# Kernel tuning notes

Measured on AMD Instinct MI355X. Metric: run time of the kernel, lower is better.

The kernel has to match this reference:

```python
import jax, jax.numpy as jnp
import numpy as np

N_COLS = 4096
N_ROWS = 4096
H = 64          # args.hidden1
S = 2           # per-edge supp feature count (cv_supp/vc_supp dim 0)
S_VO = 2        # vo_supp feature dim
S_CO = 2        # co_supp feature dim
EDGE_DENSITY = 0.03


def setup_inputs() -> dict:
    key = jax.random.key(0)
    ks = jax.random.split(key, 20)
    col_hidden = jax.random.normal(ks[0], (N_COLS, H), jnp.float32)
    row_hidden = jax.random.normal(ks[1], (N_ROWS, H), jnp.float32)
    obj_hidden = jax.random.normal(ks[2], (1, H), jnp.float32)
    # sparse bipartite adjacency encoded in supp[0] != 0 (as in the TF code)
    mask = jax.random.bernoulli(ks[3], EDGE_DENSITY, (N_ROWS, N_COLS))
    cv_supp = jax.random.normal(ks[4], (S, N_ROWS, N_COLS), jnp.float32) * mask[None]
    vc_supp = jnp.transpose(cv_supp, (0, 2, 1))  # [S, ncols, nrows]
    vo_supp = jax.random.normal(ks[5], (N_COLS, S_VO), jnp.float32)
    co_supp = jax.random.normal(ks[6], (N_ROWS, S_CO), jnp.float32)
    w = 0.05
    W_vo = jax.random.normal(ks[7], (2 * H, H), jnp.float32) * w
    W_oc = jax.random.normal(ks[8], (2 * H, H), jnp.float32) * w
    W_vc = jax.random.normal(ks[9], (2 * H, H), jnp.float32) * w
    W_co = jax.random.normal(ks[10], (2 * H, H), jnp.float32) * w
    W_ov = jax.random.normal(ks[11], (2 * H, H), jnp.float32) * w
    W_cv = jax.random.normal(ks[12], (2 * H, H), jnp.float32) * w
    # attention scorer nets: Dense(concat_dim -> 1) + sigmoid
    w_attn_vo = jax.random.normal(ks[13], (2 * H + S_VO, 1), jnp.float32) * 0.1
    b_attn_vo = jnp.zeros((), jnp.float32)
    w_attn_co = jax.random.normal(ks[14], (2 * H + S_CO, 1), jnp.float32) * 0.1
    b_attn_co = jnp.zeros((), jnp.float32)
    # pairwise attn nets decomposed into [col | supp | row] weight slices
    w_cv_col = jax.random.normal(ks[15], (H,), jnp.float32) * 0.1
    w_cv_supp = jax.random.normal(ks[16], (S,), jnp.float32) * 0.1
    w_cv_row = jax.random.normal(ks[17], (H,), jnp.float32) * 0.1
    b_cv = jnp.zeros((), jnp.float32)
    w_vc_row = jax.random.normal(ks[18], (H,), jnp.float32) * 0.1
    w_vc_supp = jax.random.normal(ks[19], (S,), jnp.float32) * 0.1
    w_vc_col = jax.random.normal(jax.random.fold_in(key, 99), (H,), jnp.float32) * 0.1
    b_vc = jnp.zeros((), jnp.float32)
    return dict(col_hidden=col_hidden, row_hidden=row_hidden, obj_hidden=obj_hidden,
                cv_supp=cv_supp, vc_supp=vc_supp, vo_supp=vo_supp, co_supp=co_supp,
                W_vo=W_vo, W_oc=W_oc, W_vc=W_vc, W_co=W_co, W_ov=W_ov, W_cv=W_cv,
                w_attn_vo=w_attn_vo, b_attn_vo=b_attn_vo,
                w_attn_co=w_attn_co, b_attn_co=b_attn_co,
                w_cv_col=w_cv_col, w_cv_supp=w_cv_supp, w_cv_row=w_cv_row, b_cv=b_cv,
                w_vc_row=w_vc_row, w_vc_supp=w_vc_supp, w_vc_col=w_vc_col, b_vc=b_vc)


def _forward(col_hidden, row_hidden, obj_hidden, cv_supp, vc_supp, vo_supp, co_supp,
             W_vo, W_oc, W_vc, W_co, W_ov, W_cv,
             w_attn_vo, b_attn_vo, w_attn_co, b_attn_co,
             w_cv_col, w_cv_supp, w_cv_row, b_cv,
             w_vc_row, w_vc_supp, w_vc_col, b_vc):
    act = jax.nn.relu
    ncols, nrows = col_hidden.shape[0], row_hidden.shape[0]
    # ---- v -> o: attend over all columns, update obj node ----
    vo_in = jnp.concatenate([col_hidden, vo_supp,
                             jnp.broadcast_to(obj_hidden, (ncols, H))], axis=1)
    a_vo = jax.nn.sigmoid(vo_in @ w_attn_vo + b_attn_vo)          # [ncols, 1]
    v_o_out = a_vo.T @ col_hidden                                  # [1, H]
    obj = act(jnp.concatenate([obj_hidden, v_o_out], axis=1) @ W_vo)
    # ---- v -> c: per-row ragged neighbor attention, vectorized via masked pairwise scores ----
    nbr_cv = cv_supp[0] != 0                                       # [nrows, ncols]
    logits_cv = ((row_hidden @ w_cv_row)[:, None]
                 + (col_hidden @ w_cv_col)[None, :]
                 + jnp.einsum('snc,s->nc', cv_supp, w_cv_supp) + b_cv)
    score_cv = jnp.where(nbr_cv, jax.nn.sigmoid(logits_cv), 0.0)   # [nrows, ncols]
    v_out = score_cv @ col_hidden                                  # [nrows, H]
    o_c_out = act(jnp.concatenate([jnp.broadcast_to(obj, (nrows, H)), row_hidden], axis=1) @ W_oc)
    row_next = act(jnp.concatenate([o_c_out, v_out], axis=1) @ W_vc)
    # ---- c -> o ----
    co_in = jnp.concatenate([row_next, co_supp,
                             jnp.broadcast_to(obj, (nrows, H))], axis=1)
    a_co = jax.nn.sigmoid(co_in @ w_attn_co + b_attn_co)           # [nrows, 1]
    c_o_out = a_co.T @ row_next                                    # [1, H]
    obj = act(jnp.concatenate([obj, c_o_out], axis=1) @ W_co)
    # ---- c -> v ----
    nbr_vc = vc_supp[0] != 0                                       # [ncols, nrows]
    logits_vc = ((col_hidden @ w_vc_col)[:, None]
                 + (row_next @ w_vc_row)[None, :]
                 + jnp.einsum('scn,s->cn', vc_supp, w_vc_supp) + b_vc)
    score_vc = jnp.where(nbr_vc, jax.nn.sigmoid(logits_vc), 0.0)   # [ncols, nrows]
    c_out = score_vc @ row_next                                    # [ncols, H]
    o_v_out = act(jnp.concatenate([jnp.broadcast_to(obj, (ncols, H)), col_hidden], axis=1) @ W_ov)
    col_next = act(jnp.concatenate([o_v_out, c_out], axis=1) @ W_cv)
    return col_next, row_next, obj


def reference(col_hidden, row_hidden, obj_hidden, cv_supp, vc_supp, vo_supp, co_supp,
              W_vo, W_oc, W_vc, W_co, W_ov, W_cv,
              w_attn_vo, b_attn_vo, w_attn_co, b_attn_co,
              w_cv_col, w_cv_supp, w_cv_row, b_cv,
              w_vc_row, w_vc_supp, w_vc_col, b_vc):
    col_next, row_next, obj = _forward(
        col_hidden, row_hidden, obj_hidden, cv_supp, vc_supp, vo_supp, co_supp,
        W_vo, W_oc, W_vc, W_co, W_ov, W_cv,
        w_attn_vo, b_attn_vo, w_attn_co, b_attn_co,
        w_cv_col, w_cv_supp, w_cv_row, b_cv,
        w_vc_row, w_vc_supp, w_vc_col, b_vc)
    # original layer also passes the supp tensors through unchanged
    return (col_next, row_next, obj, cv_supp, vc_supp, vo_supp, co_supp)
```

## Files before the change

### kernel.cpp

```cpp
#include <hip/hip_runtime.h>
#include <math.h>

typedef float f4 __attribute__((ext_vector_type(4)));

#define PLANE (4096*4096)

#define OUT_COL 0
#define OUT_ROW 262144
#define OUT_OBJ 524288
#define OUT_CV  524352
#define OUT_VC  34078784
#define OUT_VO  67633216
#define OUT_CO  67641408

#define WS_VOACC 0
#define WS_COACC 64
#define WS_OBJ1  128
#define WS_RDCV  256
#define WS_CDCV  4352
#define WS_RDVC  8448
#define WS_CDVC  12544
#define WS_VOUT  16640
#define WS_COUT  278784
#define WS_PART  540928

__device__ __forceinline__ float sigf(float x) {
    return 1.0f / (1.0f + __expf(-x));
}

__global__ __launch_bounds__(256) void k_dots(
    const float* __restrict__ col_hidden, const float* __restrict__ row_hidden,
    const float* __restrict__ w_cv_col, const float* __restrict__ w_vc_col,
    const float* __restrict__ w_cv_row,
    float* __restrict__ cdcv, float* __restrict__ cdvc, float* __restrict__ rdcv)
{
    const int gw = blockIdx.x * 4 + (threadIdx.x >> 6);
    const int lane = threadIdx.x & 63;
    const int which = gw >> 12;
    const int row = gw & 4095;
    const float* x; const float* w; float* dst;
    if (which == 0)      { x = col_hidden; w = w_cv_col; dst = cdcv; }
    else if (which == 1) { x = col_hidden; w = w_vc_col; dst = cdvc; }
    else                 { x = row_hidden; w = w_cv_row; dst = rdcv; }
    float v = x[row * 64 + lane] * w[lane];
    #pragma unroll
    for (int off = 32; off; off >>= 1) v += __shfl_down(v, off, 64);
    if (lane == 0) dst[row] = v;
}

__global__ __launch_bounds__(256) void k_attn(
    const float* __restrict__ X, const float* __restrict__ supp,
    const float* __restrict__ obj, const float* __restrict__ wat,
    const float* __restrict__ bat, float* __restrict__ accum,
    const float* __restrict__ wextra, float* __restrict__ dextra)
{
    __shared__ float sA[256];
    __shared__ float sAcc[64];
    const int t = threadIdx.x;
    const int i = blockIdx.x * 256 + t;
    float x = bat[0] + supp[i*2] * wat[64] + supp[i*2+1] * wat[65];
    float d = 0.f;
    for (int h = 0; h < 64; ++h) {
        x += obj[h] * wat[66 + h];
        float xv = X[i*64 + h];
        x += xv * wat[h];
        if (wextra) d += xv * wextra[h];
    }
    if (dextra) dextra[i] = d;
    sA[t] = sigf(x);
    if (t < 64) sAcc[t] = 0.f;
    __syncthreads();
    const int w = t >> 6, h = t & 63;
    const int base = blockIdx.x * 256 + w * 64;
    float partial = 0.f;
    for (int j = 0; j < 64; ++j)
        partial += sA[w*64 + j] * X[(base + j)*64 + h];
    atomicAdd(&sAcc[h], partial);
    __syncthreads();
    if (t < 64) atomicAdd(&accum[t], sAcc[t]);
}

__global__ void k_obj(const float* __restrict__ left, const float* __restrict__ right,
                      const float* __restrict__ W, float* __restrict__ dst)
{
    const int h = threadIdx.x;
    float acc = 0.f;
    for (int k = 0; k < 64; ++k) acc += left[k]  * W[k*64 + h];
    for (int k = 0; k < 64; ++k) acc += right[k] * W[(64+k)*64 + h];
    dst[h] = fmaxf(acc, 0.f);
}

__global__ __launch_bounds__(256) void k_big(
    const float* __restrict__ supp0, const float* __restrict__ supp1,
    const float* __restrict__ Bm,
    const float* __restrict__ rdot, const float* __restrict__ cdot,
    const float* __restrict__ wsup, const float* __restrict__ bias,
    float* __restrict__ part, float* __restrict__ pass0, float* __restrict__ pass1)
{
    __shared__ __align__(16) float sS[64][68];
    __shared__ __align__(16) float sB[64][64];
    const int t  = threadIdx.x;
    const int bi = blockIdx.x & 63;
    const int bj = blockIdx.x >> 6;
    const int i0 = bi * 64;
    const int jl4 = (t & 15) * 4;
    const int ilb = t >> 4;
    const int rgrp = ilb;
    const int h0 = jl4;
    const float w0 = wsup[0], w1 = wsup[1], bv = bias[0];

    f4 acc0 = 0.f, acc1 = 0.f, acc2 = 0.f, acc3 = 0.f;

    for (int tile = 0; tile < 8; ++tile) {
        const int jt = bj * 512 + tile * 64;
        {
            const f4* src = (const f4*)(Bm + (size_t)jt * 64);
            f4* dstp = (f4*)&sB[0][0];
            dstp[t]       = src[t];
            dstp[t + 256] = src[t + 256];
            dstp[t + 512] = src[t + 512];
            dstp[t + 768] = src[t + 768];
        }
        const f4 cd = *(const f4*)(cdot + jt + jl4);
        #pragma unroll
        for (int k = 0; k < 4; ++k) {
            const int il = ilb + 16 * k;
            const size_t idx = (size_t)(i0 + il) * 4096 + jt + jl4;
            f4 a0 = *(const f4*)(supp0 + idx);
            f4 a1 = *(const f4*)(supp1 + idx);
            *(f4*)(pass0 + idx) = a0;
            *(f4*)(pass1 + idx) = a1;
            const float rd = rdot[i0 + il];
            f4 lg = rd + cd + w0 * a0 + w1 * a1 + bv;
            f4 s;
            s.x = (a0.x != 0.f) ? sigf(lg.x) : 0.f;
            s.y = (a0.y != 0.f) ? sigf(lg.y) : 0.f;
            s.z = (a0.z != 0.f) ? sigf(lg.z) : 0.f;
            s.w = (a0.w != 0.f) ? sigf(lg.w) : 0.f;
            *(f4*)&sS[il][jl4] = s;
        }
        __syncthreads();
        #pragma unroll
        for (int jj = 0; jj < 64; jj += 4) {
            f4 b0 = *(const f4*)&sB[jj + 0][h0];
            f4 b1 = *(const f4*)&sB[jj + 1][h0];
            f4 b2 = *(const f4*)&sB[jj + 2][h0];
            f4 b3 = *(const f4*)&sB[jj + 3][h0];
            { f4 s = *(const f4*)&sS[rgrp*4 + 0][jj]; acc0 += s.x*b0 + s.y*b1 + s.z*b2 + s.w*b3; }
            { f4 s = *(const f4*)&sS[rgrp*4 + 1][jj]; acc1 += s.x*b0 + s.y*b1 + s.z*b2 + s.w*b3; }
            { f4 s = *(const f4*)&sS[rgrp*4 + 2][jj]; acc2 += s.x*b0 + s.y*b1 + s.z*b2 + s.w*b3; }
            { f4 s = *(const f4*)&sS[rgrp*4 + 3][jj]; acc3 += s.x*b0 + s.y*b1 + s.z*b2 + s.w*b3; }
        }
        __syncthreads();
    }
    float* pb = part + (size_t)bj * 262144 + (size_t)i0 * 64;
    *(f4*)(pb + (rgrp*4 + 0)*64 + h0) = acc0;
    *(f4*)(pb + (rgrp*4 + 1)*64 + h0) = acc1;
    *(f4*)(pb + (rgrp*4 + 2)*64 + h0) = acc2;
    *(f4*)(pb + (rgrp*4 + 3)*64 + h0) = acc3;
}

__global__ __launch_bounds__(256) void k_reduce(const float* __restrict__ part,
                                                float* __restrict__ dst)
{
    const int idx = blockIdx.x * 256 + threadIdx.x;
    const f4* p = (const f4*)part;
    f4 s = p[idx];
    #pragma unroll
    for (int j = 1; j < 8; ++j) s += p[j * 65536 + idx];
    ((f4*)dst)[idx] = s;
}

__global__ __launch_bounds__(256) void k_mlp2(
    const float* __restrict__ objx, const float* __restrict__ base,
    const float* __restrict__ W1, const float* __restrict__ accin,
    const float* __restrict__ W2, float* __restrict__ dst)
{
    __shared__ float mid[4][64];
    const int t = threadIdx.x, w = t >> 6, h = t & 63;
    const int n = blockIdx.x * 4 + w;
    float m = 0.f;
    for (int k = 0; k < 64; ++k) m += objx[k] * W1[k*64 + h];
    for (int k = 0; k < 64; ++k) m += base[n*64 + k] * W1[(64+k)*64 + h];
    mid[w][h] = fmaxf(m, 0.f);
    __syncthreads();
    float o = 0.f;
    for (int k = 0; k < 64; ++k) o += mid[w][k] * W2[k*64 + h];
    for (int k = 0; k < 64; ++k) o += accin[n*64 + k] * W2[(64+k)*64 + h];
    dst[n*64 + h] = fmaxf(o, 0.f);
}

__global__ void k_copy_small(const float* __restrict__ a, const float* __restrict__ b,
                             float* __restrict__ da, float* __restrict__ db)
{
    const int idx = blockIdx.x * 256 + threadIdx.x;
    if (idx < 2048) ((f4*)da)[idx] = ((const f4*)a)[idx];
    else            ((f4*)db)[idx - 2048] = ((const f4*)b)[idx - 2048];
}

extern "C" void kernel_launch(void* const* d_in, const int* in_sizes, int n_in,
                              void* d_out, int out_size, void* d_ws, size_t ws_size,
                              hipStream_t stream)
{
    const float* col_hidden = (const float*)d_in[0];
    const float* row_hidden = (const float*)d_in[1];
    const float* obj_hidden = (const float*)d_in[2];
    const float* cv_supp    = (const float*)d_in[3];
    const float* vc_supp    = (const float*)d_in[4];
    const float* vo_supp    = (const float*)d_in[5];
    const float* co_supp    = (const float*)d_in[6];
    const float* W_vo       = (const float*)d_in[7];
    const float* W_oc       = (const float*)d_in[8];
    const float* W_vc       = (const float*)d_in[9];
    const float* W_co       = (const float*)d_in[10];
    const float* W_ov       = (const float*)d_in[11];
    const float* W_cv       = (const float*)d_in[12];
    const float* w_attn_vo  = (const float*)d_in[13];
    const float* b_attn_vo  = (const float*)d_in[14];
    const float* w_attn_co  = (const float*)d_in[15];
    const float* b_attn_co  = (const float*)d_in[16];
    const float* w_cv_col   = (const float*)d_in[17];
    const float* w_cv_supp  = (const float*)d_in[18];
    const float* w_cv_row   = (const float*)d_in[19];
    const float* b_cv       = (const float*)d_in[20];
    const float* w_vc_row   = (const float*)d_in[21];
    const float* w_vc_supp  = (const float*)d_in[22];
    const float* w_vc_col   = (const float*)d_in[23];
    const float* b_vc       = (const float*)d_in[24];

    float* out = (float*)d_out;
    float* ws  = (float*)d_ws;

    hipMemsetAsync(ws, 0, 128 * sizeof(float), stream);

    k_dots<<<3072, 256, 0, stream>>>(col_hidden, row_hidden, w_cv_col, w_vc_col, w_cv_row,
                                     ws + WS_CDCV, ws + WS_CDVC, ws + WS_RDCV);
    k_attn<<<16, 256, 0, stream>>>(col_hidden, vo_supp, obj_hidden, w_attn_vo, b_attn_vo,
                                   ws + WS_VOACC, nullptr, nullptr);
    k_obj<<<1, 64, 0, stream>>>(obj_hidden, ws + WS_VOACC, W_vo, ws + WS_OBJ1);
    k_big<<<512, 256, 0, stream>>>(cv_supp, cv_supp + PLANE, col_hidden,
                                   ws + WS_RDCV, ws + WS_CDCV, w_cv_supp, b_cv,
                                   ws + WS_PART, out + OUT_CV, out + OUT_CV + PLANE);
    k_reduce<<<256, 256, 0, stream>>>(ws + WS_PART, ws + WS_VOUT);
    k_mlp2<<<1024, 256, 0, stream>>>(ws + WS_OBJ1, row_hidden, W_oc, ws + WS_VOUT, W_vc,
                                     out + OUT_ROW);
    k_attn<<<16, 256, 0, stream>>>(out + OUT_ROW, co_supp, ws + WS_OBJ1, w_attn_co, b_attn_co,
                                   ws + WS_COACC, w_vc_row, ws + WS_RDVC);
    k_obj<<<1, 64, 0, stream>>>(ws + WS_OBJ1, ws + WS_COACC, W_co, out + OUT_OBJ);
    k_big<<<512, 256, 0, stream>>>(vc_supp, vc_supp + PLANE, out + OUT_ROW,
                                   ws + WS_CDVC, ws + WS_RDVC, w_vc_supp, b_vc,
                                   ws + WS_PART, out + OUT_VC, out + OUT_VC + PLANE);
    k_reduce<<<256, 256, 0, stream>>>(ws + WS_PART, ws + WS_COUT);
    k_mlp2<<<1024, 256, 0, stream>>>(out + OUT_OBJ, col_hidden, W_ov, ws + WS_COUT, W_cv,
                                     out + OUT_COL);
    k_copy_small<<<16, 256, 0, stream>>>(vo_supp, co_supp, out + OUT_VO, out + OUT_CO);
}
```

Measured before the change: 598.6 us.

## Fuse small kernels and prefetch next tile in registers with nontemporal streaming

Merges the dot-product, small copy and first attention kernels into one front kernel, folds the obj MLP into an extra block of k_big, and folds the partial-sum reduction into k_mlp2, removing the memset and atomics to global. In k_big, the next tile's supp and B data are loaded into registers while the current tile is computed, and supp pass-through uses nontemporal loads/stores. This aims to hide memory latency on the bandwidth-bound plane streaming and cut launch overhead, at the cost of higher register pressure.

```diff
diff --git a/kernel.cpp b/kernel.cpp
--- a/kernel.cpp
+++ b/kernel.cpp
@@ -13,51 +13,27 @@
 #define OUT_VO  67633216
 #define OUT_CO  67641408
 
-#define WS_VOACC 0
-#define WS_COACC 64
-#define WS_OBJ1  128
-#define WS_RDCV  256
-#define WS_CDCV  4352
-#define WS_RDVC  8448
-#define WS_CDVC  12544
-#define WS_VOUT  16640
-#define WS_COUT  278784
-#define WS_PART  540928
+#define WS_VO_P 0
+#define WS_CO_P 1024
+#define WS_OBJ1 2048
+#define WS_RDCV 2112
+#define WS_CDCV 6208
+#define WS_RDVC 10304
+#define WS_CDVC 14400
+#define WS_PART 18496
 
 __device__ __forceinline__ float sigf(float x) {
     return 1.0f / (1.0f + __expf(-x));
 }
 
-__global__ __launch_bounds__(256) void k_dots(
-    const float* __restrict__ col_hidden, const float* __restrict__ row_hidden,
-    const float* __restrict__ w_cv_col, const float* __restrict__ w_vc_col,
-    const float* __restrict__ w_cv_row,
-    float* __restrict__ cdcv, float* __restrict__ cdvc, float* __restrict__ rdcv)
-{
-    const int gw = blockIdx.x * 4 + (threadIdx.x >> 6);
-    const int lane = threadIdx.x & 63;
-    const int which = gw >> 12;
-    const int row = gw & 4095;
-    const float* x; const float* w; float* dst;
-    if (which == 0)      { x = col_hidden; w = w_cv_col; dst = cdcv; }
-    else if (which == 1) { x = col_hidden; w = w_vc_col; dst = cdvc; }
-    else                 { x = row_hidden; w = w_cv_row; dst = rdcv; }
-    float v = x[row * 64 + lane] * w[lane];
-    #pragma unroll
-    for (int off = 32; off; off >>= 1) v += __shfl_down(v, off, 64);
-    if (lane == 0) dst[row] = v;
-}
-
-__global__ __launch_bounds__(256) void k_attn(
-    const float* __restrict__ X, const float* __restrict__ supp,
+__device__ __forceinline__ void attn_body(
+    int blk, int t, const float* __restrict__ X, const float* __restrict__ supp,
     const float* __restrict__ obj, const float* __restrict__ wat,
-    const float* __restrict__ bat, float* __restrict__ accum,
-    const float* __restrict__ wextra, float* __restrict__ dextra)
-{
-    __shared__ float sA[256];
-    __shared__ float sAcc[64];
-    const int t = threadIdx.x;
-    const int i = blockIdx.x * 256 + t;
+    const float* __restrict__ bat, float* __restrict__ accP,
+    const float* __restrict__ wextra, float* __restrict__ dextra,
+    float* sA, float* sAcc)
+{
+    const int i = blk * 256 + t;
     float x = bat[0] + supp[i*2] * wat[64] + supp[i*2+1] * wat[65];
     float d = 0.f;
     for (int h = 0; h < 64; ++h) {
@@ -71,23 +47,63 @@
     if (t < 64) sAcc[t] = 0.f;
     __syncthreads();
     const int w = t >> 6, h = t & 63;
-    const int base = blockIdx.x * 256 + w * 64;
+    const int base = blk * 256 + w * 64;
     float partial = 0.f;
     for (int j = 0; j < 64; ++j)
         partial += sA[w*64 + j] * X[(base + j)*64 + h];
     atomicAdd(&sAcc[h], partial);
     __syncthreads();
-    if (t < 64) atomicAdd(&accum[t], sAcc[t]);
-}
-
-__global__ void k_obj(const float* __restrict__ left, const float* __restrict__ right,
-                      const float* __restrict__ W, float* __restrict__ dst)
-{
-    const int h = threadIdx.x;
-    float acc = 0.f;
-    for (int k = 0; k < 64; ++k) acc += left[k]  * W[k*64 + h];
-    for (int k = 0; k < 64; ++k) acc += right[k] * W[(64+k)*64 + h];
-    dst[h] = fmaxf(acc, 0.f);
+    if (t < 64) accP[blk*64 + t] = sAcc[t];
+}
+
+__global__ __launch_bounds__(256) void k_front(
+    const float* __restrict__ col_hidden, const float* __restrict__ row_hidden,
+    const float* __restrict__ w_cv_col, const float* __restrict__ w_vc_col,
+    const float* __restrict__ w_cv_row,
+    float* __restrict__ cdcv, float* __restrict__ cdvc, float* __restrict__ rdcv,
+    const float* __restrict__ vo_supp, const float* __restrict__ co_supp,
+    float* __restrict__ out_vo, float* __restrict__ out_co,
+    const float* __restrict__ obj_hidden, const float* __restrict__ w_attn_vo,
+    const float* __restrict__ b_attn_vo, float* __restrict__ voP)
+{
+    __shared__ float sA[256];
+    __shared__ float sAcc[64];
+    const int t = threadIdx.x;
+    if (blockIdx.x < 3072) {
+        const int gw = blockIdx.x * 4 + (t >> 6);
+        const int lane = t & 63;
+        const int which = gw >> 12;
+        const int row = gw & 4095;
+        const float* x; const float* w; float* dst;
+        if (which == 0)      { x = col_hidden; w = w_cv_col; dst = cdcv; }
+        else if (which == 1) { x = col_hidden; w = w_vc_col; dst = cdvc; }
+        else                 { x = row_hidden; w = w_cv_row; dst = rdcv; }
+        float v = x[row * 64 + lane] * w[lane];
+        #pragma unroll
+        for (int off = 32; off; off >>= 1) v += __shfl_down(v, off, 64);
+        if (lane == 0) dst[row] = v;
+        return;
+    }
+    if (blockIdx.x < 3088) {
+        const int idx = (blockIdx.x - 3072) * 256 + t;
+        if (idx < 2048) ((f4*)out_vo)[idx] = ((const f4*)vo_supp)[idx];
+        else            ((f4*)out_co)[idx - 2048] = ((const f4*)co_supp)[idx - 2048];
+        return;
+    }
+    attn_body(blockIdx.x - 3088, t, col_hidden, vo_supp, obj_hidden,
+              w_attn_vo, b_attn_vo, voP, nullptr, nullptr, sA, sAcc);
+}
+
+__global__ __launch_bounds__(256) void k_attn(
+    const float* __restrict__ X, const float* __restrict__ supp,
+    const float* __restrict__ obj, const float* __restrict__ wat,
+    const float* __restrict__ bat, float* __restrict__ accP,
+    const float* __restrict__ wextra, float* __restrict__ dextra)
+{
+    __shared__ float sA[256];
+    __shared__ float sAcc[64];
+    attn_body(blockIdx.x, threadIdx.x, X, supp, obj, wat, bat, accP,
+              wextra, dextra, sA, sAcc);
 }
 
 __global__ __launch_bounds__(256) void k_big(
@@ -95,90 +111,129 @@
     const float* __restrict__ Bm,
     const float* __restrict__ rdot, const float* __restrict__ cdot,
     const float* __restrict__ wsup, const float* __restrict__ bias,
-    float* __restrict__ part, float* __restrict__ pass0, float* __restrict__ pass1)
+    float* __restrict__ part, float* __restrict__ pass0, float* __restrict__ pass1,
+    const float* __restrict__ objL, const float* __restrict__ objRp,
+    const float* __restrict__ Wobj, float* __restrict__ objDst)
 {
     __shared__ __align__(16) float sS[64][68];
     __shared__ __align__(16) float sB[64][64];
-    const int t  = threadIdx.x;
+    const int t = threadIdx.x;
+
+    if (blockIdx.x == 512) {
+        float* rsum = &sS[0][0];
+        if (t < 64) {
+            float r = 0.f;
+            for (int b = 0; b < 16; ++b) r += objRp[b*64 + t];
+            rsum[t] = r;
+        }
+        __syncthreads();
+        if (t < 64) {
+            float acc = 0.f;
+            for (int k = 0; k < 64; ++k) acc += objL[k] * Wobj[k*64 + t];
+            for (int k = 0; k < 64; ++k) acc += rsum[k] * Wobj[(64+k)*64 + t];
+            objDst[t] = fmaxf(acc, 0.f);
+        }
+        return;
+    }
+
     const int bi = blockIdx.x & 63;
     const int bj = blockIdx.x >> 6;
     const int i0 = bi * 64;
     const int jl4 = (t & 15) * 4;
     const int ilb = t >> 4;
-    const int rgrp = ilb;
-    const int h0 = jl4;
     const float w0 = wsup[0], w1 = wsup[1], bv = bias[0];
 
+    float rd[4];
+    #pragma unroll
+    for (int k = 0; k < 4; ++k) rd[k] = rdot[i0 + ilb + 16*k];
+
     f4 acc0 = 0.f, acc1 = 0.f, acc2 = 0.f, acc3 = 0.f;
-
+    f4 ca0[4], ca1[4], cb[4], ccd;
+
+    {
+        const int jt = bj * 512;
+        const f4* bsrc = (const f4*)(Bm + (size_t)jt * 64);
+        #pragma unroll
+        for (int r = 0; r < 4; ++r) cb[r] = bsrc[t + 256*r];
+        ccd = *(const f4*)(cdot + jt + jl4);
+        #pragma unroll
+        for (int k = 0; k < 4; ++k) {
+            const size_t idx = (size_t)(i0 + ilb + 16*k) * 4096 + jt + jl4;
+            ca0[k] = __builtin_nontemporal_load((const f4*)(supp0 + idx));
+            ca1[k] = __builtin_nontemporal_load((const f4*)(supp1 + idx));
+        }
+    }
+
+    #pragma unroll
     for (int tile = 0; tile < 8; ++tile) {
         const int jt = bj * 512 + tile * 64;
         {
-            const f4* src = (const f4*)(Bm + (size_t)jt * 64);
             f4* dstp = (f4*)&sB[0][0];
-            dstp[t]       = src[t];
-            dstp[t + 256] = src[t + 256];
-            dstp[t + 512] = src[t + 512];
-            dstp[t + 768] = src[t + 768];
-        }
-        const f4 cd = *(const f4*)(cdot + jt + jl4);
-        #pragma unroll
-        for (int k = 0; k < 4; ++k) {
-            const int il = ilb + 16 * k;
-            const size_t idx = (size_t)(i0 + il) * 4096 + jt + jl4;
-            f4 a0 = *(const f4*)(supp0 + idx);
-            f4 a1 = *(const f4*)(supp1 + idx);
-            *(f4*)(pass0 + idx) = a0;
-            *(f4*)(pass1 + idx) = a1;
-            const float rd = rdot[i0 + il];
-            f4 lg = rd + cd + w0 * a0 + w1 * a1 + bv;
-            f4 s;
-            s.x = (a0.x != 0.f) ? sigf(lg.x) : 0.f;
-            s.y = (a0.y != 0.f) ? sigf(lg.y) : 0.f;
-            s.z = (a0.z != 0.f) ? sigf(lg.z) : 0.f;
-            s.w = (a0.w != 0.f) ? sigf(lg.w) : 0.f;
-            *(f4*)&sS[il][jl4] = s;
+            #pragma unroll
+            for (int r = 0; r < 4; ++r) dstp[t + 256*r] = cb[r];
+            #pragma unroll
+            for (int k = 0; k < 4; ++k) {
+                const int il = ilb + 16*k;
+                const size_t idx = (size_t)(i0 + il) * 4096 + jt + jl4;
+                __builtin_nontemporal_store(ca0[k], (f4*)(pass0 + idx));
+                __builtin_nontemporal_store(ca1[k], (f4*)(pass1 + idx));
+                f4 lg = rd[k] + ccd + w0 * ca0[k] + w1 * ca1[k] + bv;
+                f4 s;
+                s.x = (ca0[k].x != 0.f) ? sigf(lg.x) : 0.f;
+                s.y = (ca0[k].y != 0.f) ? sigf(lg.y) : 0.f;
+                s.z = (ca0[k].z != 0.f) ? sigf(lg.z) : 0.f;
+                s.w = (ca0[k].w != 0.f) ? sigf(lg.w) : 0.f;
+                *(f4*)&sS[il][jl4] = s;
+            }
         }
         __syncthreads();
+        if (tile < 7) {
+            const int jn = jt + 64;
+            const f4* bsrc = (const f4*)(Bm + (size_t)jn * 64);
+            #pragma unroll
+            for (int r = 0; r < 4; ++r) cb[r] = bsrc[t + 256*r];
+            ccd = *(const f4*)(cdot + jn + jl4);
+            #pragma unroll
+            for (int k = 0; k < 4; ++k) {
+                const size_t idx = (size_t)(i0 + ilb + 16*k) * 4096 + jn + jl4;
+                ca0[k] = __builtin_nontemporal_load((const f4*)(supp0 + idx));
+                ca1[k] = __builtin_nontemporal_load((const f4*)(supp1 + idx));
+            }
+        }
+        const int h0 = jl4;
         #pragma unroll
         for (int jj = 0; jj < 64; jj += 4) {
             f4 b0 = *(const f4*)&sB[jj + 0][h0];
             f4 b1 = *(const f4*)&sB[jj + 1][h0];
             f4 b2 = *(const f4*)&sB[jj + 2][h0];
             f4 b3 = *(const f4*)&sB[jj + 3][h0];
-            { f4 s = *(const f4*)&sS[rgrp*4 + 0][jj]; acc0 += s.x*b0 + s.y*b1 + s.z*b2 + s.w*b3; }
-            { f4 s = *(const f4*)&sS[rgrp*4 + 1][jj]; acc1 += s.x*b0 + s.y*b1 + s.z*b2 + s.w*b3; }
-            { f4 s = *(const f4*)&sS[rgrp*4 + 2][jj]; acc2 += s.x*b0 + s.y*b1 + s.z*b2 + s.w*b3; }
-            { f4 s = *(const f4*)&sS[rgrp*4 + 3][jj]; acc3 += s.x*b0 + s.y*b1 + s.z*b2 + s.w*b3; }
+            { f4 s = *(const f4*)&sS[ilb*4 + 0][jj]; acc0 += s.x*b0 + s.y*b1 + s.z*b2 + s.w*b3; }
+            { f4 s = *(const f4*)&sS[ilb*4 + 1][jj]; acc1 += s.x*b0 + s.y*b1 + s.z*b2 + s.w*b3; }
+            { f4 s = *(const f4*)&sS[ilb*4 + 2][jj]; acc2 += s.x*b0 + s.y*b1 + s.z*b2 + s.w*b3; }
+            { f4 s = *(const f4*)&sS[ilb*4 + 3][jj]; acc3 += s.x*b0 + s.y*b1 + s.z*b2 + s.w*b3; }
         }
         __syncthreads();
     }
     float* pb = part + (size_t)bj * 262144 + (size_t)i0 * 64;
-    *(f4*)(pb + (rgrp*4 + 0)*64 + h0) = acc0;
-    *(f4*)(pb + (rgrp*4 + 1)*64 + h0) = acc1;
-    *(f4*)(pb + (rgrp*4 + 2)*64 + h0) = acc2;
-    *(f4*)(pb + (rgrp*4 + 3)*64 + h0) = acc3;
-}
-
-__global__ __launch_bounds__(256) void k_reduce(const float* __restrict__ part,
-                                                float* __restrict__ dst)
-{
-    const int idx = blockIdx.x * 256 + threadIdx.x;
-    const f4* p = (const f4*)part;
-    f4 s = p[idx];
-    #pragma unroll
-    for (int j = 1; j < 8; ++j) s += p[j * 65536 + idx];
-    ((f4*)dst)[idx] = s;
+    __builtin_nontemporal_store(acc0, (f4*)(pb + (ilb*4 + 0)*64 + jl4));
+    __builtin_nontemporal_store(acc1, (f4*)(pb + (ilb*4 + 1)*64 + jl4));
+    __builtin_nontemporal_store(acc2, (f4*)(pb + (ilb*4 + 2)*64 + jl4));
+    __builtin_nontemporal_store(acc3, (f4*)(pb + (ilb*4 + 3)*64 + jl4));
 }
 
 __global__ __launch_bounds__(256) void k_mlp2(
     const float* __restrict__ objx, const float* __restrict__ base,
-    const float* __restrict__ W1, const float* __restrict__ accin,
+    const float* __restrict__ W1, const float* __restrict__ part,
     const float* __restrict__ W2, float* __restrict__ dst)
 {
     __shared__ float mid[4][64];
+    __shared__ float accs[4][64];
     const int t = threadIdx.x, w = t >> 6, h = t & 63;
     const int n = blockIdx.x * 4 + w;
+    float v = 0.f;
+    #pragma unroll
+    for (int j = 0; j < 8; ++j) v += part[(size_t)j * 262144 + n*64 + h];
+    accs[w][h] = v;
     float m = 0.f;
     for (int k = 0; k < 64; ++k) m += objx[k] * W1[k*64 + h];
     for (int k = 0; k < 64; ++k) m += base[n*64 + k] * W1[(64+k)*64 + h];
@@ -186,16 +241,8 @@
     __syncthreads();
     float o = 0.f;
     for (int k = 0; k < 64; ++k) o += mid[w][k] * W2[k*64 + h];
-    for (int k = 0; k < 64; ++k) o += accin[n*64 + k] * W2[(64+k)*64 + h];
+    for (int k = 0; k < 64; ++k) o += accs[w][k] * W2[(64+k)*64 + h];
     dst[n*64 + h] = fmaxf(o, 0.f);
-}
-
-__global__ void k_copy_small(const float* __restrict__ a, const float* __restrict__ b,
-                             float* __restrict__ da, float* __restrict__ db)
-{
-    const int idx = blockIdx.x * 256 + threadIdx.x;
-    if (idx < 2048) ((f4*)da)[idx] = ((const f4*)a)[idx];
-    else            ((f4*)db)[idx - 2048] = ((const f4*)b)[idx - 2048];
 }
 
 extern "C" void kernel_launch(void* const* d_in, const int* in_sizes, int n_in,
@@ -231,27 +278,22 @@
     float* out = (float*)d_out;
     float* ws  = (float*)d_ws;
 
-    hipMemsetAsync(ws, 0, 128 * sizeof(float), stream);
-
-    k_dots<<<3072, 256, 0, stream>>>(col_hidden, row_hidden, w_cv_col, w_vc_col, w_cv_row,
-                                     ws + WS_CDCV, ws + WS_CDVC, ws + WS_RDCV);
-    k_attn<<<16, 256, 0, stream>>>(col_hidden, vo_supp, obj_hidden, w_attn_vo, b_attn_vo,
-                                   ws + WS_VOACC, nullptr, nullptr);
-    k_obj<<<1, 64, 0, stream>>>(obj_hidden, ws + WS_VOACC, W_vo, ws + WS_OBJ1);
-    k_big<<<512, 256, 0, stream>>>(cv_supp, cv_supp + PLANE, col_hidden,
+    k_front<<<3104, 256, 0, stream>>>(col_hidden, row_hidden, w_cv_col, w_vc_col, w_cv_row,
+                                      ws + WS_CDCV, ws + WS_CDVC, ws + WS_RDCV,
+                                      vo_supp, co_supp, out + OUT_VO, out + OUT_CO,
+                                      obj_hidden, w_attn_vo, b_attn_vo, ws + WS_VO_P);
+    k_big<<<513, 256, 0, stream>>>(cv_supp, cv_supp + PLANE, col_hidden,
                                    ws + WS_RDCV, ws + WS_CDCV, w_cv_supp, b_cv,
-                                   ws + WS_PART, out + OUT_CV, out + OUT_CV + PLANE);
-    k_reduce<<<256, 256, 0, stream>>>(ws + WS_PART, ws + WS_VOUT);
-    k_mlp2<<<1024, 256, 0, stream>>>(ws + WS_OBJ1, row_hidden, W_oc, ws + WS_VOUT, W_vc,
+                                   ws + WS_PART, out + OUT_CV, out + OUT_CV + PLANE,
+                                   obj_hidden, ws + WS_VO_P, W_vo, ws + WS_OBJ1);
+    k_mlp2<<<1024, 256, 0, stream>>>(ws + WS_OBJ1, row_hidden, W_oc, ws + WS_PART, W_vc,
                                      out + OUT_ROW);
     k_attn<<<16, 256, 0, stream>>>(out + OUT_ROW, co_supp, ws + WS_OBJ1, w_attn_co, b_attn_co,
-                                   ws + WS_COACC, w_vc_row, ws + WS_RDVC);
-    k_obj<<<1, 64, 0, stream>>>(ws + WS_OBJ1, ws + WS_COACC, W_co, out + OUT_OBJ);
-    k_big<<<512, 256, 0, stream>>>(vc_supp, vc_supp + PLANE, out + OUT_ROW,
+                                   ws + WS_CO_P, w_vc_row, ws + WS_RDVC);
+    k_big<<<513, 256, 0, stream>>>(vc_supp, vc_supp + PLANE, out + OUT_ROW,
                                    ws + WS_CDVC, ws + WS_RDVC, w_vc_supp, b_vc,
-                                   ws + WS_PART, out + OUT_VC, out + OUT_VC + PLANE);
-    k_reduce<<<256, 256, 0, stream>>>(ws + WS_PART, ws + WS_COUT);
-    k_mlp2<<<1024, 256, 0, stream>>>(out + OUT_OBJ, col_hidden, W_ov, ws + WS_COUT, W_cv,
+                                   ws + WS_PART, out + OUT_VC, out + OUT_VC + PLANE,
+                                   ws + WS_OBJ1, ws + WS_CO_P, W_co, out + OUT_OBJ);
+    k_mlp2<<<1024, 256, 0, stream>>>(out + OUT_OBJ, col_hidden, W_ov, ws + WS_PART, W_cv,
                                      out + OUT_COL);
-    k_copy_small<<<16, 256, 0, stream>>>(vo_supp, co_supp, out + OUT_VO, out + OUT_CO);
-}
+}
```

Result: slower. 2.068 ms (+245.5%).
